# Kernel tuning notes

Measured on AMD Instinct MI355X. Metric: run time of the kernel, lower is better.

## Reference

```python
import jax, jax.numpy as jnp
import numpy as np

B, S, E, H = 4, 1024, 1024, 16
HD = E // H
SCALE = HD ** -0.5


def setup_inputs() -> dict:
    key = jax.random.key(0)
    ks = jax.random.split(key, 10)
    std = E ** -0.5
    return {
        "sequence_embeddings": jax.random.normal(ks[0], (B, S, E), jnp.float32),
        "graph_embeddings": jax.random.normal(ks[1], (B, S, HD), jnp.float32),
        "Wq": jax.random.normal(ks[2], (E, E), jnp.float32) * std,
        "bq": jnp.zeros((E,), jnp.float32),
        "Wk": jax.random.normal(ks[3], (E, E), jnp.float32) * std,
        "bk": jnp.zeros((E,), jnp.float32),
        "Wv": jax.random.normal(ks[4], (E, E), jnp.float32) * std,
        "bv": jnp.zeros((E,), jnp.float32),
        "Wo": jax.random.normal(ks[5], (E, E), jnp.float32) * std,
        "bo": jnp.zeros((E,), jnp.float32),
    }


def reference(sequence_embeddings, graph_embeddings, Wq, bq, Wk, bk, Wv, bv, Wo, bo):
    b, s, e = sequence_embeddings.shape
    # project and split heads: [b, h, s, hd]
    def heads(x, W, bias):
        return (x @ W + bias).reshape(b, s, H, HD).transpose(0, 2, 1, 3)

    q = heads(sequence_embeddings, Wq, bq)
    k = heads(sequence_embeddings, Wk, bk)
    v = heads(sequence_embeddings, Wv, bv)

    # sequence-to-sequence attention: [b, h, s, s]
    attn_scores = jnp.einsum("bhqd,bhkd->bhqk", q, k) * SCALE
    seq_attn = jax.nn.softmax(attn_scores, axis=-1)

    # graph-to-sequence attention: graph [b, s, hd] broadcast over heads -> [b, h, s, s]
    graph_scores = jnp.einsum("bqd,bhkd->bhqk", graph_embeddings, k)
    graph_attn = jax.nn.softmax(graph_scores, axis=-1)

    # fused dual-softmax weights (dropout is identity in eval)
    attn_weights = seq_attn * graph_attn

    attn_out = jnp.einsum("bhqk,bhkd->bhqd", attn_weights, v)
    attn_out = attn_out.transpose(0, 2, 1, 3).reshape(b, s, e)
    output = attn_out @ Wo + bo
    return output, attn_weights
```

## Files before the change

### kernel.cpp

```cpp
#include <hip/hip_runtime.h>
#include <math.h>

#define B_ 4
#define S_ 1024
#define E_ 1024
#define H_ 16
#define HD_ 64

#define LOG2E 1.4426950408889634f
#define C16L2 23.08312065422341f
#define C64L2 92.33248261689365f
#define C80L2 115.41560327111706f

typedef float4 f4;
typedef _Float16 f16x8 __attribute__((ext_vector_type(8)));
typedef ushort u16x8 __attribute__((ext_vector_type(8)));
typedef float f32x4 __attribute__((ext_vector_type(4)));

__device__ __forceinline__ void gl16(const void* g, void* l) {
  __builtin_amdgcn_global_load_lds(
      (__attribute__((address_space(1))) void*)g,
      (__attribute__((address_space(3))) void*)l, 16, 0, 0);
}

__device__ __forceinline__ ushort f2h(float x) {
  return __builtin_bit_cast(ushort, (_Float16)x);
}
__device__ __forceinline__ float h2f(ushort h) {
  return (float)__builtin_bit_cast(_Float16, h);
}
__device__ __forceinline__ float exp2r(float x) {
  return __builtin_amdgcn_exp2f(x);
}
__device__ __forceinline__ f32x4 mfma16(u16x8 a, u16x8 b, f32x4 c) {
  return __builtin_amdgcn_mfma_f32_16x16x32_f16(
      __builtin_bit_cast(f16x8, a), __builtin_bit_cast(f16x8, b), c, 0, 0, 0);
}
__device__ __forceinline__ u16x8 ldfrag(const ushort* s, int row, int chunk) {
  return *reinterpret_cast<const u16x8*>(s + row * 64 + ((chunk ^ (row & 7)) << 3));
}


__global__ __launch_bounds__(256) void prep_x(
    const float* __restrict__ x, ushort* __restrict__ xf)
{
  const size_t i = ((size_t)blockIdx.x * 256 + threadIdx.x) * 8;
  float v[8];
  *reinterpret_cast<f4*>(v)     = *reinterpret_cast<const f4*>(x + i);
  *reinterpret_cast<f4*>(v + 4) = *reinterpret_cast<const f4*>(x + i + 4);
  unsigned fw[4];
#pragma unroll
  for (int p = 0; p < 4; ++p)
    fw[p] = (unsigned)f2h(v[2 * p]) | ((unsigned)f2h(v[2 * p + 1]) << 16);
  *reinterpret_cast<uint4*>(xf + i) = make_uint4(fw[0], fw[1], fw[2], fw[3]);
}

__global__ __launch_bounds__(256) void prep_w(
    const float* __restrict__ Wq, const float* __restrict__ Wk,
    const float* __restrict__ Wv, const float* __restrict__ Wo,
    ushort* __restrict__ ws16)
{
  const int MSZ = 1024 * 1024;
  const int mat = blockIdx.z;
  const int n0 = blockIdx.x * 64, k0 = blockIdx.y * 64;
  const float* W = mat == 0 ? Wq : mat == 1 ? Wk : mat == 2 ? Wv : Wo;
  ushort* Oh = ws16 + (size_t)mat * MSZ;

  __shared__ __align__(16) float tile[64][65];
  const int t = threadIdx.x;
  const int r = t >> 2, cq = t & 3;
#pragma unroll
  for (int j = 0; j < 4; ++j) {
    const f4 v = *reinterpret_cast<const f4*>(&W[(size_t)(k0 + r) * 1024 + n0 + cq * 16 + 4 * j]);
    tile[r][cq * 16 + 4 * j + 0] = v.x;
    tile[r][cq * 16 + 4 * j + 1] = v.y;
    tile[r][cq * 16 + 4 * j + 2] = v.z;
    tile[r][cq * 16 + 4 * j + 3] = v.w;
  }
  __syncthreads();
  unsigned hw[8];
#pragma unroll
  for (int p = 0; p < 8; ++p)
    hw[p] = (unsigned)f2h(tile[cq * 16 + 2 * p][r]) |
            ((unsigned)f2h(tile[cq * 16 + 2 * p + 1][r]) << 16);
  ushort* dh = Oh + (size_t)(n0 + r) * 1024 + k0 + cq * 16;
  *reinterpret_cast<uint4*>(dh)     = make_uint4(hw[0], hw[1], hw[2], hw[3]);
  *reinterpret_cast<uint4*>(dh + 8) = make_uint4(hw[4], hw[5], hw[6], hw[7]);
}

template <int OMODE>
__global__ __launch_bounds__(256) void gemm_mfma(
    const ushort* __restrict__ Ab, const ushort* __restrict__ Bhg,
    const float* __restrict__ bias, float scale,
    ushort* __restrict__ Oh, float* __restrict__ Of)
{
  const int n0 = blockIdx.x * 128;
  const int m0 = blockIdx.y * 64;
  const int t = threadIdx.x;
  const int wv = t >> 6, lane = t & 63;
  const int lr = lane & 15, lg = lane >> 4;
  const int wm = (wv >> 1) * 32, wn = (wv & 1) * 64;
  const int row8 = lane >> 3, ch8 = lane & 7;

  __shared__ __align__(16) ushort Ah_s[64 * 64];
  __shared__ __align__(16) ushort Bh_s[128 * 64];
  __shared__ __align__(16) ushort tr_s[OMODE == 2 ? 128 * 72 : 16];

  f32x4 acc[2][4];
#pragma unroll
  for (int mi = 0; mi < 2; ++mi)
#pragma unroll
    for (int ni = 0; ni < 4; ++ni) { f32x4 z = {0.f, 0.f, 0.f, 0.f}; acc[mi][ni] = z; }

  for (int kt = 0; kt < 16; ++kt) {
    const int k0 = kt * 64;
    __syncthreads();
#pragma unroll
    for (int j = 0; j < 4; ++j) {
      const int row = wv * 32 + j * 8 + row8;
      gl16(Bhg + (size_t)(n0 + row) * 1024 + k0 + ((ch8 ^ (row & 7)) << 3),
           &Bh_s[(wv * 32 + j * 8) * 64]);
    }
#pragma unroll
    for (int j = 0; j < 2; ++j) {
      const int row = wv * 16 + j * 8 + row8;
      gl16(Ab + (size_t)(m0 + row) * 1024 + k0 + ((ch8 ^ (row & 7)) << 3),
           &Ah_s[(wv * 16 + j * 8) * 64]);
    }
    __syncthreads();
#pragma unroll
    for (int ks = 0; ks < 2; ++ks) {
      const u16x8 ah0 = ldfrag(Ah_s, wm + lr, ks * 4 + lg);
      const u16x8 ah1 = ldfrag(Ah_s, wm + 16 + lr, ks * 4 + lg);
#pragma unroll
      for (int ni = 0; ni < 4; ++ni) {
        const u16x8 bh = ldfrag(Bh_s, wn + ni * 16 + lr, ks * 4 + lg);
        acc[0][ni] = mfma16(ah0, bh, acc[0][ni]);
        acc[1][ni] = mfma16(ah1, bh, acc[1][ni]);
      }
    }
  }

  if constexpr (OMODE == 2) {
    __syncthreads();
#pragma unroll
    for (int mi = 0; mi < 2; ++mi)
#pragma unroll
      for (int ni = 0; ni < 4; ++ni)
#pragma unroll
        for (int r = 0; r < 4; ++r) {
          const int n_l = wn + ni * 16 + lr, m_l = wm + mi * 16 + lg * 4 + r;
          tr_s[n_l * 72 + m_l] = f2h(acc[mi][ni][r] + bias[n0 + n_l]);
        }
    __syncthreads();
    const int row = t >> 1, hf = t & 1;
    const int n_g = n0 + row;
    const int h_ = n_g >> 6, hd = n_g & 63;
    const int b_g = m0 >> 10;
    ushort* dst = Oh + ((size_t)(b_g * 16 + h_) * 64 + hd) * 1024 + (m0 & 1023) + hf * 32;
#pragma unroll
    for (int j = 0; j < 4; ++j)
      *reinterpret_cast<uint4*>(dst + 8 * j) =
          *reinterpret_cast<const uint4*>(&tr_s[row * 72 + hf * 32 + 8 * j]);
  } else {
#pragma unroll
    for (int mi = 0; mi < 2; ++mi)
#pragma unroll
      for (int ni = 0; ni < 4; ++ni) {
        const int n = n0 + wn + ni * 16 + lr;
        const float bi = bias[n];
#pragma unroll
        for (int r = 0; r < 4; ++r) {
          const int m = m0 + wm + mi * 16 + lg * 4 + r;
          const float v = (acc[mi][ni][r] + bi) * scale;
          if constexpr (OMODE == 0) {
            Of[(size_t)m * 1024 + n] = v;
          } else {
            const size_t addr =
                ((size_t)((m >> 10) * 16 + (n >> 6)) * 1024 + (m & 1023)) * 64 + (n & 63);
            Oh[addr] = f2h(v);
          }
        }
      }
  }
}

__global__ __launch_bounds__(256) void attn_mfma(
    const ushort* __restrict__ qh_g, const ushort* __restrict__ kf_g,
    const ushort* __restrict__ vt_g, const float* __restrict__ ge,
    float* __restrict__ attn, ushort* __restrict__ aoh)
{
  __shared__ __align__(16) ushort kh2_s[2][4096];
  __shared__ __align__(16) ushort vt2_s[2][4096];

  const int bid = blockIdx.x;
  const int wg = (bid & 7) * 128 + (bid >> 3);
  const int bh = wg >> 4, qb = wg & 15;
  const int b = bh >> 4, h = bh & 15;

  const int t = threadIdx.x;
  const int wv = t >> 6, lane = t & 63;
  const int lr = lane & 15, lg = lane >> 4;
  const int q0 = qb * 64 + wv * 16;

  u16x8 qh[2], gh[2];
  float gf[2][8];
#pragma unroll
  for (int ks = 0; ks < 2; ++ks) {
    const size_t qoff = ((size_t)bh * S_ + q0 + lr) * HD_ + ks * 32 + lg * 8;
    qh[ks] = *reinterpret_cast<const u16x8*>(qh_g + qoff);
    const float* grow = ge + ((size_t)b * S_ + q0 + lr) * HD_ + ks * 32 + lg * 8;
    f4 g0 = *reinterpret_cast<const f4*>(grow);
    f4 g1 = *reinterpret_cast<const f4*>(grow + 4);
    gf[ks][0] = g0.x * LOG2E; gf[ks][1] = g0.y * LOG2E;
    gf[ks][2] = g0.z * LOG2E; gf[ks][3] = g0.w * LOG2E;
    gf[ks][4] = g1.x * LOG2E; gf[ks][5] = g1.y * LOG2E;
    gf[ks][6] = g1.z * LOG2E; gf[ks][7] = g1.w * LOG2E;
#pragma unroll
    for (int e = 0; e < 8; ++e) gh[ks][e] = f2h(gf[ks][e]);
  }

  const ushort* kfb = kf_g + (size_t)bh * S_ * HD_;
  const ushort* vtb = vt_g + (size_t)bh * HD_ * S_;

  const int srow = t >> 2;
  const int sc0 = t & 3;
  auto stage_kf = [&](int kt, int c) {
#pragma unroll
    for (int j = 0; j < 2; ++j) {
      const int ch = sc0 + j * 4;
      gl16(kfb + kt * 4096 + srow * 64 + ((ch ^ (srow & 7)) << 3),
           &kh2_s[c][(srow & 56) * 64 + (srow & 7) * 128 + j * 64]);
    }
  };
  auto stage_vt = [&](int kt, int c) {
#pragma unroll
    for (int j = 0; j < 2; ++j) {
      const int ch = sc0 + j * 4;
      gl16(vtb + kt * 64 + (size_t)srow * 1024 + ((ch ^ (srow & 7)) << 3),
           &vt2_s[c][(srow & 56) * 64 + (srow & 7) * 128 + j * 64]);
    }
  };

  const int krow = wv * 16 + (lane >> 2);
  const int kch0 = lane & 3;
  auto stage_k2 = [&](int kt, int c) {
#pragma unroll
    for (int j = 0; j < 2; ++j) {
      const int ch = kch0 + j * 4;
      gl16(kfb + kt * 4096 + krow * 64 + (((ch) ^ (krow & 7)) << 3),
           &kh2_s[c][(wv * 16) * 64 + (lane >> 2) * 0 + j * 2048 + 0]);
    }
  };
  (void)stage_kf; (void)stage_vt; (void)stage_k2;

  auto stage_K = [&](int kt, int c) {
#pragma unroll
    for (int j = 0; j < 2; ++j) {
      const int row = wv * 16 + (lane >> 2);
      const int ch = j * 4 + (lane & 3);
      gl16(kfb + kt * 4096 + row * 64 + ((ch ^ (row & 7)) << 3),
           &kh2_s[c][j * 2048 + (wv * 16) * 32]);
    }
  };
  auto stage_V = [&](int kt, int c) {
#pragma unroll
    for (int j = 0; j < 2; ++j) {
      const int row = wv * 16 + (lane >> 2);
      const int ch = j * 4 + (lane & 3);
      gl16(vtb + kt * 64 + (size_t)row * 1024 + ((ch ^ (row & 7)) << 3),
           &vt2_s[c][j * 2048 + (wv * 16) * 32]);
    }
  };
  auto ldfragH = [&](const ushort* s, int row, int ch) -> u16x8 {
    const int chx = ch ^ (row & 7);
    return *reinterpret_cast<const u16x8*>(
        s + (chx >> 2) * 2048 + row * 32 + (chx & 3) * 8);
  };

  float z1L = 0.f, z2L = 0.f;

  asm volatile("s_waitcnt vmcnt(0)" ::: "memory");
  __builtin_amdgcn_sched_barrier(0);

  stage_K(0, 0);
  for (int kt = 0; kt < 16; ++kt) {
    if (kt < 15) {
      stage_K(kt + 1, (kt + 1) & 1);
      asm volatile("s_waitcnt vmcnt(2)" ::: "memory");
    } else {
      asm volatile("s_waitcnt vmcnt(0)" ::: "memory");
    }
    __builtin_amdgcn_sched_barrier(0);
    __builtin_amdgcn_s_barrier();
    __builtin_amdgcn_sched_barrier(0);

    const ushort* kp = kh2_s[kt & 1];
    f32x4 s1[4], s2[4];
    __builtin_amdgcn_s_setprio(1);
#pragma unroll
    for (int ct = 0; ct < 4; ++ct) {
      f32x4 z = {0.f, 0.f, 0.f, 0.f};
      s1[ct] = z; s2[ct] = z;
#pragma unroll
      for (int ks = 0; ks < 2; ++ks) {
        const u16x8 kA = ldfragH(kp, ct * 16 + lr, ks * 4 + lg);
        s1[ct] = mfma16(kA, qh[ks], s1[ct]);
        s2[ct] = mfma16(kA, gh[ks], s2[ct]);
      }
    }
    __builtin_amdgcn_s_setprio(0);
#pragma unroll
    for (int ct = 0; ct < 4; ++ct)
#pragma unroll
      for (int r = 0; r < 4; ++r) {
        z1L += exp2r(s1[ct][r] - C16L2);
        z2L += exp2r(s2[ct][r] - C64L2);
      }
    __builtin_amdgcn_s_barrier();
    __builtin_amdgcn_sched_barrier(0);
  }

  float z1 = z1L + __shfl_xor(z1L, 16);
  z1 += __shfl_xor(z1, 32);
  float z2 = z2L + __shfl_xor(z2L, 16);
  z2 += __shfl_xor(z2, 32);
  const float rz = 1.f / (z1 * z2);

  stage_K(0, 0);
  stage_V(0, 0);

  u16x8 uh[2];
#pragma unroll
  for (int ks = 0; ks < 2; ++ks)
#pragma unroll
    for (int e = 0; e < 8; ++e)
      uh[ks][e] = f2h(h2f(qh[ks][e]) + gf[ks][e]);

  f32x4 o[4];
#pragma unroll
  for (int dt = 0; dt < 4; ++dt) { f32x4 z = {0.f, 0.f, 0.f, 0.f}; o[dt] = z; }

  float* wrow = attn + ((size_t)bh * S_ + q0) * S_;
  const int prowBase = ((lr >> 2) << 3) | (lr & 3);

  for (int kt = 0; kt < 16; ++kt) {
    if (kt < 15) {
      stage_K(kt + 1, (kt + 1) & 1);
      stage_V(kt + 1, (kt + 1) & 1);
      if (kt == 0) asm volatile("s_waitcnt vmcnt(4)" ::: "memory");
      else         asm volatile("s_waitcnt vmcnt(8)" ::: "memory");
    } else {
      asm volatile("s_waitcnt vmcnt(4)" ::: "memory");
    }
    __builtin_amdgcn_sched_barrier(0);
    __builtin_amdgcn_s_barrier();
    __builtin_amdgcn_sched_barrier(0);

    const int c = kt & 1;
    const ushort* kfp = kh2_s[c];
    const ushort* vtp = vt2_s[c];

#pragma unroll
    for (int hf = 0; hf < 2; ++hf) {
      f32x4 s12[2];
      {
        f32x4 z = {0.f, 0.f, 0.f, 0.f};
        s12[0] = z; s12[1] = z;
      }
      __builtin_amdgcn_s_setprio(1);
#pragma unroll
      for (int ks = 0; ks < 2; ++ks) {
        const u16x8 kA0 = ldfragH(kfp, hf * 32 + prowBase, ks * 4 + lg);
        const u16x8 kA1 = ldfragH(kfp, hf * 32 + (prowBase | 4), ks * 4 + lg);
        s12[0] = mfma16(kA0, uh[ks], s12[0]);
        s12[1] = mfma16(kA1, uh[ks], s12[1]);
      }
      __builtin_amdgcn_s_setprio(0);

      float wv2[8];
      u16x8 af;
#pragma unroll
      for (int ct = 0; ct < 2; ++ct)
#pragma unroll
        for (int r = 0; r < 4; ++r) {
          const float w = exp2r(s12[ct][r] - C80L2) * rz;
          wv2[ct * 4 + r] = w;
          af[ct * 4 + r] = f2h(w);
        }

      __builtin_amdgcn_s_setprio(1);
#pragma unroll
      for (int dt = 0; dt < 4; ++dt) {
        const u16x8 vf = ldfragH(vtp, dt * 16 + lr, hf * 4 + lg);
        o[dt] = mfma16(af, vf, o[dt]);
      }
      __builtin_amdgcn_s_setprio(0);

      {
        float* dst = wrow + (size_t)lr * S_ + kt * 64 + hf * 32 + lg * 8;
        *reinterpret_cast<f4*>(dst)     = make_float4(wv2[0], wv2[1], wv2[2], wv2[3]);
        *reinterpret_cast<f4*>(dst + 4) = make_float4(wv2[4], wv2[5], wv2[6], wv2[7]);
      }
    }
    __builtin_amdgcn_s_barrier();
    __builtin_amdgcn_sched_barrier(0);
  }

#pragma unroll
  for (int dt = 0; dt < 4; ++dt)
#pragma unroll
    for (int r = 0; r < 4; ++r)
      aoh[((size_t)b * S_ + q0 + lg * 4 + r) * E_ + h * 64 + dt * 16 + lr] =
          f2h(o[dt][r]);
}

extern "C" void kernel_launch(void* const* d_in, const int* in_sizes, int n_in,
                              void* d_out, int out_size, void* d_ws, size_t ws_size,
                              hipStream_t stream) {
  const float* x  = (const float*)d_in[0];
  const float* ge = (const float*)d_in[1];
  const float* Wq = (const float*)d_in[2];
  const float* bq = (const float*)d_in[3];
  const float* Wk = (const float*)d_in[4];
  const float* bk = (const float*)d_in[5];
  const float* Wv = (const float*)d_in[6];
  const float* bv = (const float*)d_in[7];
  const float* Wo = (const float*)d_in[8];
  const float* bo = (const float*)d_in[9];

  float* out  = (float*)d_out;
  float* attn = out + (size_t)B_ * S_ * E_;

  const size_t MSZ = 1024 * 1024;
  ushort* ws16 = (ushort*)d_ws;
  ushort* Wqf = ws16 + 0 * MSZ;
  ushort* Wkf = ws16 + 1 * MSZ;
  ushort* Wvf = ws16 + 2 * MSZ;
  ushort* Wof = ws16 + 3 * MSZ;
  ushort* xf  = ws16 + 4 * MSZ;
  ushort* qh  = ws16 + 8 * MSZ;
  ushort* kf  = ws16 + 12 * MSZ;
  ushort* vt  = ws16 + 16 * MSZ;
  ushort* aoh = ws16 + 20 * MSZ;

  dim3 blk(256);
  hipLaunchKernelGGL(prep_x, dim3(2048), blk, 0, stream, x, xf);
  hipLaunchKernelGGL(prep_w, dim3(16, 16, 4), blk, 0, stream, Wq, Wk, Wv, Wo, ws16);

  dim3 ggrid(E_ / 128, (B_ * S_) / 64);
  hipLaunchKernelGGL((gemm_mfma<3>), ggrid, blk, 0, stream,
                     xf, Wqf, bq, 0.125f * LOG2E, qh, nullptr);
  hipLaunchKernelGGL((gemm_mfma<3>), ggrid, blk, 0, stream,
                     xf, Wkf, bk, 1.0f, kf, nullptr);
  hipLaunchKernelGGL((gemm_mfma<2>), ggrid, blk, 0, stream,
                     xf, Wvf, bv, 1.0f, vt, nullptr);

  hipLaunchKernelGGL(attn_mfma, dim3(1024), blk, 0, stream,
                     qh, kf, vt, ge, attn, aoh);

  hipLaunchKernelGGL((gemm_mfma<0>), ggrid, blk, 0, stream,
                     aoh, Wof, bo, 1.0f, nullptr, out);
}
```

Measured before the change: 176.9 us.

## Merge Q/K projection GEMMs into one launch and use larger K tiles in pass one

The Q and K projection GEMMs now run as a single launch that uses a z grid dimension to select weights, bias and output. The separate shared buffers in the attention kernel become one shared array. The first pass over K (the softmax normalisers) now stages 128-row K tiles in 8 iterations instead of 64-row tiles in 16, halving the barrier count there. The intent is to cut launch overhead and sync cost, at the price of more registers for the larger score arrays and use of an `ldfrag` helper with a different layout than the `ldfragH` used for the other staging.

After: 156.1 us. -11.8%, faster.

```diff
diff --git a/kernel.cpp b/kernel.cpp
--- a/kernel.cpp
+++ b/kernel.cpp
@@ -89,22 +89,17 @@
 }
 
 template <int OMODE>
-__global__ __launch_bounds__(256) void gemm_mfma(
+__device__ __forceinline__ void gemm_body(
     const ushort* __restrict__ Ab, const ushort* __restrict__ Bhg,
     const float* __restrict__ bias, float scale,
-    ushort* __restrict__ Oh, float* __restrict__ Of)
-{
-  const int n0 = blockIdx.x * 128;
-  const int m0 = blockIdx.y * 64;
+    ushort* __restrict__ Oh, float* __restrict__ Of,
+    int n0, int m0, ushort* Ah_s, ushort* Bh_s, ushort* tr_s)
+{
   const int t = threadIdx.x;
   const int wv = t >> 6, lane = t & 63;
   const int lr = lane & 15, lg = lane >> 4;
   const int wm = (wv >> 1) * 32, wn = (wv & 1) * 64;
   const int row8 = lane >> 3, ch8 = lane & 7;
-
-  __shared__ __align__(16) ushort Ah_s[64 * 64];
-  __shared__ __align__(16) ushort Bh_s[128 * 64];
-  __shared__ __align__(16) ushort tr_s[OMODE == 2 ? 128 * 72 : 16];
 
   f32x4 acc[2][4];
 #pragma unroll
@@ -185,13 +180,39 @@
   }
 }
 
+template <int OMODE>
+__global__ __launch_bounds__(256) void gemm_mfma(
+    const ushort* __restrict__ Ab, const ushort* __restrict__ Bhg,
+    const float* __restrict__ bias, float scale,
+    ushort* __restrict__ Oh, float* __restrict__ Of)
+{
+  __shared__ __align__(16) ushort Ah_s[64 * 64];
+  __shared__ __align__(16) ushort Bh_s[128 * 64];
+  __shared__ __align__(16) ushort tr_s[OMODE == 2 ? 128 * 72 : 16];
+  gemm_body<OMODE>(Ab, Bhg, bias, scale, Oh, Of,
+                   blockIdx.x * 128, blockIdx.y * 64, Ah_s, Bh_s, tr_s);
+}
+
+__global__ __launch_bounds__(256) void gemm_qk(
+    const ushort* __restrict__ Ab,
+    const ushort* __restrict__ Bq, const ushort* __restrict__ Bk,
+    const float* __restrict__ bq, const float* __restrict__ bk,
+    float sq, float sk,
+    ushort* __restrict__ Oq, ushort* __restrict__ Ok)
+{
+  __shared__ __align__(16) ushort Ah_s[64 * 64];
+  __shared__ __align__(16) ushort Bh_s[128 * 64];
+  const int z = blockIdx.z;
+  gemm_body<3>(Ab, z ? Bk : Bq, z ? bk : bq, z ? sk : sq, z ? Ok : Oq, nullptr,
+               blockIdx.x * 128, blockIdx.y * 64, Ah_s, Bh_s, nullptr);
+}
+
 __global__ __launch_bounds__(256) void attn_mfma(
     const ushort* __restrict__ qh_g, const ushort* __restrict__ kf_g,
     const ushort* __restrict__ vt_g, const float* __restrict__ ge,
     float* __restrict__ attn, ushort* __restrict__ aoh)
 {
-  __shared__ __align__(16) ushort kh2_s[2][4096];
-  __shared__ __align__(16) ushort vt2_s[2][4096];
+  __shared__ __align__(16) ushort smem[16384];
 
   const int bid = blockIdx.x;
   const int wg = (bid & 7) * 128 + (bid >> 3);
@@ -201,6 +222,7 @@
   const int t = threadIdx.x;
   const int wv = t >> 6, lane = t & 63;
   const int lr = lane & 15, lg = lane >> 4;
+  const int row8 = lane >> 3, ch8 = lane & 7;
   const int q0 = qb * 64 + wv * 16;
 
   u16x8 qh[2], gh[2];
@@ -223,44 +245,21 @@
   const ushort* kfb = kf_g + (size_t)bh * S_ * HD_;
   const ushort* vtb = vt_g + (size_t)bh * HD_ * S_;
 
-  const int srow = t >> 2;
-  const int sc0 = t & 3;
-  auto stage_kf = [&](int kt, int c) {
-#pragma unroll
-    for (int j = 0; j < 2; ++j) {
-      const int ch = sc0 + j * 4;
-      gl16(kfb + kt * 4096 + srow * 64 + ((ch ^ (srow & 7)) << 3),
-           &kh2_s[c][(srow & 56) * 64 + (srow & 7) * 128 + j * 64]);
+  auto stage_K1 = [&](int kt, int c) {
+#pragma unroll
+    for (int j = 0; j < 4; ++j) {
+      const int row = wv * 32 + j * 8 + row8;
+      gl16(kfb + (size_t)kt * 8192 + row * 64 + ((ch8 ^ (row & 7)) << 3),
+           &smem[c * 8192 + (wv * 32 + j * 8) * 64]);
     }
   };
-  auto stage_vt = [&](int kt, int c) {
-#pragma unroll
-    for (int j = 0; j < 2; ++j) {
-      const int ch = sc0 + j * 4;
-      gl16(vtb + kt * 64 + (size_t)srow * 1024 + ((ch ^ (srow & 7)) << 3),
-           &vt2_s[c][(srow & 56) * 64 + (srow & 7) * 128 + j * 64]);
-    }
-  };
-
-  const int krow = wv * 16 + (lane >> 2);
-  const int kch0 = lane & 3;
-  auto stage_k2 = [&](int kt, int c) {
-#pragma unroll
-    for (int j = 0; j < 2; ++j) {
-      const int ch = kch0 + j * 4;
-      gl16(kfb + kt * 4096 + krow * 64 + (((ch) ^ (krow & 7)) << 3),
-           &kh2_s[c][(wv * 16) * 64 + (lane >> 2) * 0 + j * 2048 + 0]);
-    }
-  };
-  (void)stage_kf; (void)stage_vt; (void)stage_k2;
-
   auto stage_K = [&](int kt, int c) {
 #pragma unroll
     for (int j = 0; j < 2; ++j) {
       const int row = wv * 16 + (lane >> 2);
       const int ch = j * 4 + (lane & 3);
-      gl16(kfb + kt * 4096 + row * 64 + ((ch ^ (row & 7)) << 3),
-           &kh2_s[c][j * 2048 + (wv * 16) * 32]);
+      gl16(kfb + (size_t)kt * 4096 + row * 64 + ((ch ^ (row & 7)) << 3),
+           &smem[c * 4096 + j * 2048 + (wv * 16) * 32]);
     }
   };
   auto stage_V = [&](int kt, int c) {
@@ -268,8 +267,8 @@
     for (int j = 0; j < 2; ++j) {
       const int row = wv * 16 + (lane >> 2);
       const int ch = j * 4 + (lane & 3);
-      gl16(vtb + kt * 64 + (size_t)row * 1024 + ((ch ^ (row & 7)) << 3),
-           &vt2_s[c][j * 2048 + (wv * 16) * 32]);
+      gl16(vtb + (size_t)kt * 64 + (size_t)row * 1024 + ((ch ^ (row & 7)) << 3),
+           &smem[8192 + c * 4096 + j * 2048 + (wv * 16) * 32]);
     }
   };
   auto ldfragH = [&](const ushort* s, int row, int ch) -> u16x8 {
@@ -283,11 +282,11 @@
   asm volatile("s_waitcnt vmcnt(0)" ::: "memory");
   __builtin_amdgcn_sched_barrier(0);
 
-  stage_K(0, 0);
-  for (int kt = 0; kt < 16; ++kt) {
-    if (kt < 15) {
-      stage_K(kt + 1, (kt + 1) & 1);
-      asm volatile("s_waitcnt vmcnt(2)" ::: "memory");
+  stage_K1(0, 0);
+  for (int kt = 0; kt < 8; ++kt) {
+    if (kt < 7) {
+      stage_K1(kt + 1, (kt + 1) & 1);
+      asm volatile("s_waitcnt vmcnt(4)" ::: "memory");
     } else {
       asm volatile("s_waitcnt vmcnt(0)" ::: "memory");
     }
@@ -295,23 +294,23 @@
     __builtin_amdgcn_s_barrier();
     __builtin_amdgcn_sched_barrier(0);
 
-    const ushort* kp = kh2_s[kt & 1];
-    f32x4 s1[4], s2[4];
+    const ushort* kp = smem + (kt & 1) * 8192;
     __builtin_amdgcn_s_setprio(1);
-#pragma unroll
-    for (int ct = 0; ct < 4; ++ct) {
+    f32x4 s1[8], s2[8];
+#pragma unroll
+    for (int ct = 0; ct < 8; ++ct) {
       f32x4 z = {0.f, 0.f, 0.f, 0.f};
       s1[ct] = z; s2[ct] = z;
 #pragma unroll
       for (int ks = 0; ks < 2; ++ks) {
-        const u16x8 kA = ldfragH(kp, ct * 16 + lr, ks * 4 + lg);
+        const u16x8 kA = ldfrag(kp, ct * 16 + lr, ks * 4 + lg);
         s1[ct] = mfma16(kA, qh[ks], s1[ct]);
         s2[ct] = mfma16(kA, gh[ks], s2[ct]);
       }
     }
     __builtin_amdgcn_s_setprio(0);
 #pragma unroll
-    for (int ct = 0; ct < 4; ++ct)
+    for (int ct = 0; ct < 8; ++ct)
 #pragma unroll
       for (int r = 0; r < 4; ++r) {
         z1L += exp2r(s1[ct][r] - C16L2);
@@ -358,8 +357,8 @@
     __builtin_amdgcn_sched_barrier(0);
 
     const int c = kt & 1;
-    const ushort* kfp = kh2_s[c];
-    const ushort* vtp = vt2_s[c];
+    const ushort* kfp = smem + c * 4096;
+    const ushort* vtp = smem + 8192 + c * 4096;
 
 #pragma unroll
     for (int hf = 0; hf < 2; ++hf) {
@@ -448,17 +447,14 @@
   hipLaunchKernelGGL(prep_x, dim3(2048), blk, 0, stream, x, xf);
   hipLaunchKernelGGL(prep_w, dim3(16, 16, 4), blk, 0, stream, Wq, Wk, Wv, Wo, ws16);
 
-  dim3 ggrid(E_ / 128, (B_ * S_) / 64);
-  hipLaunchKernelGGL((gemm_mfma<3>), ggrid, blk, 0, stream,
-                     xf, Wqf, bq, 0.125f * LOG2E, qh, nullptr);
-  hipLaunchKernelGGL((gemm_mfma<3>), ggrid, blk, 0, stream,
-                     xf, Wkf, bk, 1.0f, kf, nullptr);
-  hipLaunchKernelGGL((gemm_mfma<2>), ggrid, blk, 0, stream,
+  hipLaunchKernelGGL(gemm_qk, dim3(E_ / 128, (B_ * S_) / 64, 2), blk, 0, stream,
+                     xf, Wqf, Wkf, bq, bk, 0.125f * LOG2E, 1.0f, qh, kf);
+  hipLaunchKernelGGL((gemm_mfma<2>), dim3(E_ / 128, (B_ * S_) / 64), blk, 0, stream,
                      xf, Wvf, bv, 1.0f, vt, nullptr);
 
   hipLaunchKernelGGL(attn_mfma, dim3(1024), blk, 0, stream,
                      qh, kf, vt, ge, attn, aoh);
 
-  hipLaunchKernelGGL((gemm_mfma<0>), ggrid, blk, 0, stream,
+  hipLaunchKernelGGL((gemm_mfma<0>), dim3(E_ / 128, (B_ * S_) / 64), blk, 0, stream,
                      aoh, Wof, bo, 1.0f, nullptr, out);
 }
```
